# Kernel tuning notes

Hardware: AMD Instinct MI355X
Metric: run time of the kernel (lower is better)

Reference implementation:

```python
import jax, jax.numpy as jnp
import numpy as np

LN_EPS = 1e-5  # torch LayerNorm default
K_NN = 5       # top-5 nearest patterns (simple-surprise path)


def setup_inputs() -> dict:
    key = jax.random.key(0)
    ks = jax.random.split(key, 5)
    B, S, D, M = 8, 8192, 256, 50
    return {
        "hidden_states": jax.random.normal(ks[0], (B, S, D), dtype=jnp.float32),
        "memory": jax.random.normal(ks[1], (M, D), dtype=jnp.float32),
        "W1": jax.random.normal(ks[2], (D, 2 * D), dtype=jnp.float32) * (1.0 / np.sqrt(D)),
        "b1": jnp.zeros((2 * D,), dtype=jnp.float32),
        "W2": jax.random.normal(ks[3], (2 * D, D), dtype=jnp.float32) * (1.0 / np.sqrt(2 * D)),
        "b2": jnp.zeros((D,), dtype=jnp.float32),
        "ln_gamma": jnp.ones((D,), dtype=jnp.float32),
        "ln_beta": jnp.zeros((D,), dtype=jnp.float32),
    }


def reference(hidden_states, memory, W1, b1, W2, b2, ln_gamma, ln_beta):
    # Feature extractor: Linear -> ReLU -> (Dropout, eval=identity) -> Linear -> LayerNorm
    h = jax.nn.relu(jnp.einsum("bsd,de->bse", hidden_states, W1) + b1)
    f = jnp.einsum("bse,ed->bsd", h, W2) + b2
    mu = jnp.mean(f, axis=-1, keepdims=True)
    var = jnp.var(f, axis=-1, keepdims=True)
    feats = (f - mu) * jax.lax.rsqrt(var + LN_EPS) * ln_gamma + ln_beta  # [B,S,D]

    # Simple-surprise path, vectorized over all (b, s) tokens:
    # L2 distance of each token feature to every memory pattern.
    f_sq = jnp.sum(feats * feats, axis=-1)      # [B,S]
    m_sq = jnp.sum(memory * memory, axis=-1)    # [M]
    dots = jnp.einsum("bsd,md->bsm", feats, memory)  # [B,S,M]
    d2 = jnp.maximum(f_sq[..., None] + m_sq - 2.0 * dots, 0.0)
    dists = jnp.sqrt(d2)                        # [B,S,M]

    # k smallest distances -> mean -> sigmoid(avg - 1)
    neg_knn, _ = jax.lax.top_k(-dists, K_NN)    # [B,S,K]
    avg_dist = -jnp.mean(neg_knn, axis=-1)      # [B,S]
    surprise_scores = jax.nn.sigmoid(avg_dist - 1.0)
    return surprise_scores
```

## Files before the change

kernel.cpp:

```cpp
#include <hip/hip_runtime.h>
#include <math.h>

typedef __attribute__((ext_vector_type(8))) short bf16x8;
typedef __attribute__((ext_vector_type(4))) float f32x4;

static __device__ __forceinline__ unsigned int cvtpk(float lo, float hi) {
  unsigned int r;
  asm("v_cvt_pk_bf16_f32 %0, %1, %2" : "=v"(r) : "v"(lo), "v"(hi));
  return r;
}

__global__ void prep_weights(const float* __restrict__ W1,
                             const float* __restrict__ W2,
                             const float* __restrict__ mem,
                             unsigned short* __restrict__ W1T,
                             unsigned short* __restrict__ W2T,
                             unsigned short* __restrict__ memB,
                             float* __restrict__ msq) {
  const int bid = blockIdx.x, tid = threadIdx.x;
  if (bid < 64) {
    __shared__ float tile[64][65];
    const float* src;
    unsigned short* dst;
    int C, Cd, k0, n0;
    if (bid < 32) {
      src = W1; dst = W1T; C = 512; Cd = 256;
      k0 = (bid >> 3) * 64; n0 = (bid & 7) * 64;
    } else {
      int t = bid - 32;
      src = W2; dst = W2T; C = 256; Cd = 512;
      k0 = (t >> 2) * 64; n0 = (t & 3) * 64;
    }
    int r = tid >> 2, c4 = (tid & 3) * 16;
    const float4* s4 = (const float4*)(src + (k0 + r) * C + n0 + c4);
#pragma unroll
    for (int j = 0; j < 4; ++j) {
      float4 v = s4[j];
      tile[r][c4 + j * 4 + 0] = v.x;
      tile[r][c4 + j * 4 + 1] = v.y;
      tile[r][c4 + j * 4 + 2] = v.z;
      tile[r][c4 + j * 4 + 3] = v.w;
    }
    __syncthreads();
    int nl = tid >> 2, kq = (tid & 3) * 16;
    unsigned int o[8];
#pragma unroll
    for (int j = 0; j < 8; ++j)
      o[j] = cvtpk(tile[kq + 2 * j][nl], tile[kq + 2 * j + 1][nl]);
    unsigned short* dp = dst + (n0 + nl) * Cd + k0 + kq;
    *(uint4*)(dp) = make_uint4(o[0], o[1], o[2], o[3]);
    *(uint4*)(dp + 8) = make_uint4(o[4], o[5], o[6], o[7]);
  } else if (bid == 64) {
    int j0 = tid * 64;
#pragma unroll
    for (int j = 0; j < 16; ++j) {
      int e = j0 + j * 4;
      int rrow = e >> 8;
      uint2 w;
      if (rrow < 50) {
        float4 v = *(const float4*)(mem + e);
        w = make_uint2(cvtpk(v.x, v.y), cvtpk(v.z, v.w));
      } else {
        w = make_uint2(0u, 0u);
      }
      *(uint2*)(memB + e) = w;
    }
  } else {
    int rrow = tid >> 2, c0 = (tid & 3) * 64;
    float s = 0.f;
    if (rrow < 50) {
      const float4* m4 = (const float4*)(mem + rrow * 256 + c0);
#pragma unroll
      for (int c = 0; c < 16; ++c) {
        float4 v = m4[c];
        s += v.x * v.x + v.y * v.y + v.z * v.z + v.w * v.w;
      }
    }
    s += __shfl_xor(s, 1, 64);
    s += __shfl_xor(s, 2, 64);
    if ((tid & 3) == 0) msq[rrow] = (rrow < 50) ? s : 1e30f;
  }
}

#define DPitch 53
#define SWZ(b, r) ((b) ^ (((r) & 7) << 4))

__global__ __launch_bounds__(512, 4) void fused_main(
    const float* __restrict__ X, const float* __restrict__ b1v,
    const float* __restrict__ b2v, const float* __restrict__ gammav,
    const float* __restrict__ betav, const unsigned short* __restrict__ W1T,
    const unsigned short* __restrict__ W2T,
    const unsigned short* __restrict__ memB, const float* __restrict__ msq,
    float* __restrict__ out) {
  __shared__ __align__(16) char smem[65536];
  float* distS = (float*)smem;
  float* red = (float*)(smem + 32768);
  float* psum   = red;
  float* psumsq = red + 512;
  float* fsqp   = red + 1024;
  float* muS    = red + 1536;
  float* rstdS  = red + 1600;
  float* fsqS   = red + 1664;

  const char* W1Tc = (const char*)W1T;
  const char* W2Tc = (const char*)W2T;

  const int tid = threadIdx.x;
  const int wid = tid >> 6;
  const int lane = tid & 63;
  const int l16 = lane & 15;
  const int quad = lane >> 4;

  const float4* X4 = (const float4*)(X + (size_t)blockIdx.x * 64 * 256);
#pragma unroll
  for (int j = 0; j < 8; ++j) {
    int row = j * 8 + wid;
    float4 v = X4[row * 64 + lane];
    *(uint2*)(smem + SWZ(row * 512 + lane * 8, row)) =
        make_uint2(cvtpk(v.x, v.y), cvtpk(v.z, v.w));
  }

  f32x4 acc2[2][4];
#pragma unroll
  for (int mt = 0; mt < 2; ++mt) {
    const float4 bb = *(const float4*)(&b2v[wid * 32 + mt * 16 + quad * 4]);
#pragma unroll
    for (int nt = 0; nt < 4; ++nt) {
      acc2[mt][nt][0] = bb.x; acc2[mt][nt][1] = bb.y;
      acc2[mt][nt][2] = bb.z; acc2[mt][nt][3] = bb.w;
    }
  }

  __syncthreads();

#pragma unroll
  for (int cc = 0; cc < 4; ++cc) {
    if (cc > 0) {
      const char* HsR = smem + 32768 + ((cc - 1) & 1) * 16384;
#pragma unroll
      for (int k2 = 0; k2 < 4; ++k2) {
        bf16x8 a[2], b[4];
#pragma unroll
        for (int mt = 0; mt < 2; ++mt)
          a[mt] = *(const bf16x8*)(W2Tc + (wid * 32 + mt * 16 + l16) * 1024 +
                                   (cc - 1) * 256 + k2 * 64 + quad * 16);
#pragma unroll
        for (int nt = 0; nt < 4; ++nt) {
          int r = nt * 16 + l16;
          b[nt] = *(const bf16x8*)(HsR + SWZ(r * 256 + k2 * 64 + quad * 16, r));
        }
#pragma unroll
        for (int mt = 0; mt < 2; ++mt)
#pragma unroll
          for (int nt = 0; nt < 4; ++nt)
            acc2[mt][nt] = __builtin_amdgcn_mfma_f32_16x16x32_bf16(
                a[mt], b[nt], acc2[mt][nt], 0, 0, 0);
      }
    }

    int hbase = cc * 128 + wid * 16;
    f32x4 acc1[4];
    {
      const float4 bb = *(const float4*)(&b1v[hbase + quad * 4]);
#pragma unroll
      for (int nt = 0; nt < 4; ++nt) {
        acc1[nt][0] = bb.x; acc1[nt][1] = bb.y;
        acc1[nt][2] = bb.z; acc1[nt][3] = bb.w;
      }
    }
#pragma unroll
    for (int kk = 0; kk < 8; ++kk) {
      int kb = kk * 64 + quad * 16;
      bf16x8 a = *(const bf16x8*)(W1Tc + (hbase + l16) * 512 + kb);
      bf16x8 b[4];
#pragma unroll
      for (int nt = 0; nt < 4; ++nt) {
        int r = nt * 16 + l16;
        b[nt] = *(const bf16x8*)(smem + SWZ(r * 512 + kb, r));
      }
#pragma unroll
      for (int nt = 0; nt < 4; ++nt)
        acc1[nt] = __builtin_amdgcn_mfma_f32_16x16x32_bf16(a, b[nt], acc1[nt], 0, 0, 0);
    }
    {
      char* HsW = smem + 32768 + (cc & 1) * 16384;
#pragma unroll
      for (int nt = 0; nt < 4; ++nt) {
        int token = nt * 16 + l16;
        f32x4 v = acc1[nt];
        *(uint2*)(HsW + SWZ(token * 256 + wid * 32 + quad * 8, token)) =
            make_uint2(cvtpk(fmaxf(v[0], 0.f), fmaxf(v[1], 0.f)),
                       cvtpk(fmaxf(v[2], 0.f), fmaxf(v[3], 0.f)));
      }
    }
    __syncthreads();
  }

  {
    const char* HsR = smem + 32768 + 16384;
#pragma unroll
    for (int k2 = 0; k2 < 4; ++k2) {
      bf16x8 a[2], b[4];
#pragma unroll
      for (int mt = 0; mt < 2; ++mt)
        a[mt] = *(const bf16x8*)(W2Tc + (wid * 32 + mt * 16 + l16) * 1024 +
                                 3 * 256 + k2 * 64 + quad * 16);
#pragma unroll
      for (int nt = 0; nt < 4; ++nt) {
        int r = nt * 16 + l16;
        b[nt] = *(const bf16x8*)(HsR + SWZ(r * 256 + k2 * 64 + quad * 16, r));
      }
#pragma unroll
      for (int mt = 0; mt < 2; ++mt)
#pragma unroll
        for (int nt = 0; nt < 4; ++nt)
          acc2[mt][nt] = __builtin_amdgcn_mfma_f32_16x16x32_bf16(
              a[mt], b[nt], acc2[mt][nt], 0, 0, 0);
    }
  }

#pragma unroll
  for (int nt = 0; nt < 4; ++nt) {
    float s = 0.f, sq = 0.f;
#pragma unroll
    for (int mt = 0; mt < 2; ++mt)
#pragma unroll
      for (int r = 0; r < 4; ++r) {
        float v = acc2[mt][nt][r];
        s += v; sq += v * v;
      }
    s += __shfl_xor(s, 16, 64); sq += __shfl_xor(sq, 16, 64);
    s += __shfl_xor(s, 32, 64); sq += __shfl_xor(sq, 32, 64);
    if (quad == 0) {
      psum[wid * 64 + nt * 16 + l16] = s;
      psumsq[wid * 64 + nt * 16 + l16] = sq;
    }
  }
  __syncthreads();
  if (tid < 64) {
    float s = 0.f, sq = 0.f;
#pragma unroll
    for (int w = 0; w < 8; ++w) {
      s += psum[w * 64 + tid];
      sq += psumsq[w * 64 + tid];
    }
    float mu = s * (1.f / 256.f);
    float var = sq * (1.f / 256.f) - mu * mu;
    muS[tid] = mu;
    rstdS[tid] = rsqrtf(var + 1e-5f);
  }
  __syncthreads();

  {
    float4 g[2], be_[2];
#pragma unroll
    for (int mt = 0; mt < 2; ++mt) {
      g[mt]   = *(const float4*)(&gammav[wid * 32 + mt * 16 + quad * 4]);
      be_[mt] = *(const float4*)(&betav[wid * 32 + mt * 16 + quad * 4]);
    }
#pragma unroll
    for (int nt = 0; nt < 4; ++nt) {
      int token = nt * 16 + l16;
      float mu = muS[token], rs = rstdS[token];
      float fs = 0.f;
#pragma unroll
      for (int mt = 0; mt < 2; ++mt) {
        float y0 = (acc2[mt][nt][0] - mu) * rs * g[mt].x + be_[mt].x;
        float y1 = (acc2[mt][nt][1] - mu) * rs * g[mt].y + be_[mt].y;
        float y2 = (acc2[mt][nt][2] - mu) * rs * g[mt].z + be_[mt].z;
        float y3 = (acc2[mt][nt][3] - mu) * rs * g[mt].w + be_[mt].w;
        fs += y0 * y0 + y1 * y1 + y2 * y2 + y3 * y3;
        *(uint2*)(smem + SWZ(token * 512 + wid * 64 + mt * 32 + quad * 8, token)) =
            make_uint2(cvtpk(y0, y1), cvtpk(y2, y3));
      }
      fs += __shfl_xor(fs, 16, 64);
      fs += __shfl_xor(fs, 32, 64);
      if (quad == 0) fsqp[wid * 64 + token] = fs;
    }
  }
  __syncthreads();
  if (tid < 64) {
    float fs = 0.f;
#pragma unroll
    for (int w = 0; w < 8; ++w) fs += fsqp[w * 64 + tid];
    fsqS[tid] = fs;
  }
  __syncthreads();

  {
    const int th = wid & 3, mh = wid >> 2;
    f32x4 acc3[2];
#pragma unroll
    for (int j = 0; j < 2; ++j) {
      acc3[j][0] = 0.f; acc3[j][1] = 0.f; acc3[j][2] = 0.f; acc3[j][3] = 0.f;
    }
    const int ar = th * 16 + l16;
#pragma unroll
    for (int kk = 0; kk < 8; ++kk) {
      int kb = kk * 64 + quad * 16;
      bf16x8 a = *(const bf16x8*)(smem + SWZ(ar * 512 + kb, ar));
      int k0 = kk * 32 + quad * 8;
#pragma unroll
      for (int j = 0; j < 2; ++j) {
        bf16x8 b = *(const bf16x8*)(memB + (mh * 32 + j * 16 + l16) * 256 + k0);
        acc3[j] = __builtin_amdgcn_mfma_f32_16x16x32_bf16(a, b, acc3[j], 0, 0, 0);
      }
    }
    __syncthreads();
    float4 fsq4 = *(const float4*)(&fsqS[th * 16 + quad * 4]);
#pragma unroll
    for (int j = 0; j < 2; ++j) {
      int col = mh * 32 + j * 16 + l16;
      float mq = msq[col];
#pragma unroll
      for (int r = 0; r < 4; ++r) {
        float fv = (r == 0) ? fsq4.x : (r == 1) ? fsq4.y : (r == 2) ? fsq4.z : fsq4.w;
        float d2 = fv + mq - 2.f * acc3[j][r];
        float d = sqrtf(fmaxf(d2, 0.f));
        int row = th * 16 + quad * 4 + r;
        if (col < 50) distS[row * DPitch + col] = d;
      }
    }
  }
  __syncthreads();

  if (tid < 64) {
    float b0 = 1e30f, b1 = 1e30f, b2 = 1e30f, b3 = 1e30f, b4 = 1e30f;
    const float* dr = &distS[tid * DPitch];
    for (int j = 0; j < 50; ++j) {
      float v = dr[j];
      b4 = fminf(b4, v);
      float t;
      if (b4 < b3) { t = b3; b3 = b4; b4 = t; }
      if (b3 < b2) { t = b2; b2 = b3; b3 = t; }
      if (b2 < b1) { t = b1; b1 = b2; b2 = t; }
      if (b1 < b0) { t = b0; b0 = b1; b1 = t; }
    }
    float avg = (b0 + b1 + b2 + b3 + b4) * 0.2f;
    float sarg = avg - 1.f;
    out[blockIdx.x * 64 + tid] = 1.f / (1.f + __expf(-sarg));
  }
}

extern "C" void kernel_launch(void* const* d_in, const int* in_sizes, int n_in,
                              void* d_out, int out_size, void* d_ws, size_t ws_size,
                              hipStream_t stream) {
  const float* X   = (const float*)d_in[0];
  const float* mem = (const float*)d_in[1];
  const float* W1  = (const float*)d_in[2];
  const float* b1  = (const float*)d_in[3];
  const float* W2  = (const float*)d_in[4];
  const float* b2  = (const float*)d_in[5];
  const float* g   = (const float*)d_in[6];
  const float* be  = (const float*)d_in[7];
  float* out = (float*)d_out;

  unsigned short* W1T  = (unsigned short*)d_ws;
  unsigned short* W2T  = W1T + 131072;
  unsigned short* memB = W2T + 131072;
  float* msq = (float*)(memB + 16384);

  prep_weights<<<66, 256, 0, stream>>>(W1, W2, mem, W1T, W2T, memB, msq);
  fused_main<<<1024, 512, 0, stream>>>(X, b1, b2, g, be, W1T, W2T, memB, msq, out);
}
```

Baseline: 194.2 us.

## Use 4 waves per block with larger per-wave MFMA tiles and prefetched W2

Halves the block to 256 threads so each wave computes twice as many output rows in both GEMMs, which raises operand reuse per LDS load. W2 fragments for each chunk are loaded into registers ahead of the first GEMM, and the second GEMM now runs right after the barrier of the same chunk, with s_setprio raised around it. The separate reduction steps for LayerNorm stats and feature norms are folded into the consumers, removing two barriers. This costs much higher register pressure (a 64-register W2 prefetch plus larger accumulators) and fewer waves per CU, which could reduce latency hiding.

After: 214.2 us. 1.1x slower.

```diff
diff --git a/kernel.cpp b/kernel.cpp
--- a/kernel.cpp
+++ b/kernel.cpp
@@ -85,7 +85,7 @@
 #define DPitch 53
 #define SWZ(b, r) ((b) ^ (((r) & 7) << 4))
 
-__global__ __launch_bounds__(512, 4) void fused_main(
+__global__ __launch_bounds__(256, 2) void fused_main(
     const float* __restrict__ X, const float* __restrict__ b1v,
     const float* __restrict__ b2v, const float* __restrict__ gammav,
     const float* __restrict__ betav, const unsigned short* __restrict__ W1T,
@@ -96,11 +96,8 @@
   float* distS = (float*)smem;
   float* red = (float*)(smem + 32768);
   float* psum   = red;
-  float* psumsq = red + 512;
-  float* fsqp   = red + 1024;
-  float* muS    = red + 1536;
-  float* rstdS  = red + 1600;
-  float* fsqS   = red + 1664;
+  float* psumsq = red + 256;
+  float* fsqp   = red + 512;
 
   const char* W1Tc = (const char*)W1T;
   const char* W2Tc = (const char*)W2T;
@@ -113,17 +110,17 @@
 
   const float4* X4 = (const float4*)(X + (size_t)blockIdx.x * 64 * 256);
 #pragma unroll
-  for (int j = 0; j < 8; ++j) {
-    int row = j * 8 + wid;
+  for (int j = 0; j < 16; ++j) {
+    int row = j * 4 + wid;
     float4 v = X4[row * 64 + lane];
     *(uint2*)(smem + SWZ(row * 512 + lane * 8, row)) =
         make_uint2(cvtpk(v.x, v.y), cvtpk(v.z, v.w));
   }
 
-  f32x4 acc2[2][4];
-#pragma unroll
-  for (int mt = 0; mt < 2; ++mt) {
-    const float4 bb = *(const float4*)(&b2v[wid * 32 + mt * 16 + quad * 4]);
+  f32x4 acc2[4][4];
+#pragma unroll
+  for (int mt = 0; mt < 4; ++mt) {
+    const float4 bb = *(const float4*)(&b2v[wid * 64 + mt * 16 + quad * 4]);
 #pragma unroll
     for (int nt = 0; nt < 4; ++nt) {
       acc2[mt][nt][0] = bb.x; acc2[mt][nt][1] = bb.y;
@@ -135,87 +132,77 @@
 
 #pragma unroll
   for (int cc = 0; cc < 4; ++cc) {
-    if (cc > 0) {
-      const char* HsR = smem + 32768 + ((cc - 1) & 1) * 16384;
+    bf16x8 a2p[4][4];
+#pragma unroll
+    for (int k2 = 0; k2 < 4; ++k2)
+#pragma unroll
+      for (int mt = 0; mt < 4; ++mt)
+        a2p[k2][mt] = *(const bf16x8*)(W2Tc + (wid * 64 + mt * 16 + l16) * 1024 +
+                                       cc * 256 + k2 * 64 + quad * 16);
+
+    int hbase = cc * 128 + wid * 32;
+    f32x4 acc1[2][4];
+#pragma unroll
+    for (int mt = 0; mt < 2; ++mt) {
+      const float4 bb = *(const float4*)(&b1v[hbase + mt * 16 + quad * 4]);
+#pragma unroll
+      for (int nt = 0; nt < 4; ++nt) {
+        acc1[mt][nt][0] = bb.x; acc1[mt][nt][1] = bb.y;
+        acc1[mt][nt][2] = bb.z; acc1[mt][nt][3] = bb.w;
+      }
+    }
+#pragma unroll
+    for (int kk = 0; kk < 8; ++kk) {
+      int kb = kk * 64 + quad * 16;
+      bf16x8 a[2], b[4];
+#pragma unroll
+      for (int mt = 0; mt < 2; ++mt)
+        a[mt] = *(const bf16x8*)(W1Tc + (hbase + mt * 16 + l16) * 512 + kb);
+#pragma unroll
+      for (int nt = 0; nt < 4; ++nt) {
+        int r = nt * 16 + l16;
+        b[nt] = *(const bf16x8*)(smem + SWZ(r * 512 + kb, r));
+      }
+#pragma unroll
+      for (int mt = 0; mt < 2; ++mt)
+#pragma unroll
+        for (int nt = 0; nt < 4; ++nt)
+          acc1[mt][nt] = __builtin_amdgcn_mfma_f32_16x16x32_bf16(
+              a[mt], b[nt], acc1[mt][nt], 0, 0, 0);
+    }
+    {
+      char* HsW = smem + 32768 + (cc & 1) * 16384;
+#pragma unroll
+      for (int mt = 0; mt < 2; ++mt)
+#pragma unroll
+        for (int nt = 0; nt < 4; ++nt) {
+          int token = nt * 16 + l16;
+          f32x4 v = acc1[mt][nt];
+          *(uint2*)(HsW + SWZ(token * 256 + wid * 64 + mt * 32 + quad * 8, token)) =
+              make_uint2(cvtpk(fmaxf(v[0], 0.f), fmaxf(v[1], 0.f)),
+                         cvtpk(fmaxf(v[2], 0.f), fmaxf(v[3], 0.f)));
+        }
+    }
+    __syncthreads();
+    {
+      const char* HsR = smem + 32768 + (cc & 1) * 16384;
+      __builtin_amdgcn_s_setprio(1);
 #pragma unroll
       for (int k2 = 0; k2 < 4; ++k2) {
-        bf16x8 a[2], b[4];
-#pragma unroll
-        for (int mt = 0; mt < 2; ++mt)
-          a[mt] = *(const bf16x8*)(W2Tc + (wid * 32 + mt * 16 + l16) * 1024 +
-                                   (cc - 1) * 256 + k2 * 64 + quad * 16);
+        bf16x8 b[4];
 #pragma unroll
         for (int nt = 0; nt < 4; ++nt) {
           int r = nt * 16 + l16;
           b[nt] = *(const bf16x8*)(HsR + SWZ(r * 256 + k2 * 64 + quad * 16, r));
         }
 #pragma unroll
-        for (int mt = 0; mt < 2; ++mt)
+        for (int mt = 0; mt < 4; ++mt)
 #pragma unroll
           for (int nt = 0; nt < 4; ++nt)
             acc2[mt][nt] = __builtin_amdgcn_mfma_f32_16x16x32_bf16(
-                a[mt], b[nt], acc2[mt][nt], 0, 0, 0);
-      }
-    }
-
-    int hbase = cc * 128 + wid * 16;
-    f32x4 acc1[4];
-    {
-      const float4 bb = *(const float4*)(&b1v[hbase + quad * 4]);
-#pragma unroll
-      for (int nt = 0; nt < 4; ++nt) {
-        acc1[nt][0] = bb.x; acc1[nt][1] = bb.y;
-        acc1[nt][2] = bb.z; acc1[nt][3] = bb.w;
-      }
-    }
-#pragma unroll
-    for (int kk = 0; kk < 8; ++kk) {
-      int kb = kk * 64 + quad * 16;
-      bf16x8 a = *(const bf16x8*)(W1Tc + (hbase + l16) * 512 + kb);
-      bf16x8 b[4];
-#pragma unroll
-      for (int nt = 0; nt < 4; ++nt) {
-        int r = nt * 16 + l16;
-        b[nt] = *(const bf16x8*)(smem + SWZ(r * 512 + kb, r));
-      }
-#pragma unroll
-      for (int nt = 0; nt < 4; ++nt)
-        acc1[nt] = __builtin_amdgcn_mfma_f32_16x16x32_bf16(a, b[nt], acc1[nt], 0, 0, 0);
-    }
-    {
-      char* HsW = smem + 32768 + (cc & 1) * 16384;
-#pragma unroll
-      for (int nt = 0; nt < 4; ++nt) {
-        int token = nt * 16 + l16;
-        f32x4 v = acc1[nt];
-        *(uint2*)(HsW + SWZ(token * 256 + wid * 32 + quad * 8, token)) =
-            make_uint2(cvtpk(fmaxf(v[0], 0.f), fmaxf(v[1], 0.f)),
-                       cvtpk(fmaxf(v[2], 0.f), fmaxf(v[3], 0.f)));
-      }
-    }
-    __syncthreads();
-  }
-
-  {
-    const char* HsR = smem + 32768 + 16384;
-#pragma unroll
-    for (int k2 = 0; k2 < 4; ++k2) {
-      bf16x8 a[2], b[4];
-#pragma unroll
-      for (int mt = 0; mt < 2; ++mt)
-        a[mt] = *(const bf16x8*)(W2Tc + (wid * 32 + mt * 16 + l16) * 1024 +
-                                 3 * 256 + k2 * 64 + quad * 16);
-#pragma unroll
-      for (int nt = 0; nt < 4; ++nt) {
-        int r = nt * 16 + l16;
-        b[nt] = *(const bf16x8*)(HsR + SWZ(r * 256 + k2 * 64 + quad * 16, r));
-      }
-#pragma unroll
-      for (int mt = 0; mt < 2; ++mt)
-#pragma unroll
-        for (int nt = 0; nt < 4; ++nt)
-          acc2[mt][nt] = __builtin_amdgcn_mfma_f32_16x16x32_bf16(
-              a[mt], b[nt], acc2[mt][nt], 0, 0, 0);
+                a2p[k2][mt], b[nt], acc2[mt][nt], 0, 0, 0);
+      }
+      __builtin_amdgcn_s_setprio(0);
     }
   }
 
@@ -223,7 +210,7 @@
   for (int nt = 0; nt < 4; ++nt) {
     float s = 0.f, sq = 0.f;
 #pragma unroll
-    for (int mt = 0; mt < 2; ++mt)
+    for (int mt = 0; mt < 4; ++mt)
 #pragma unroll
       for (int r = 0; r < 4; ++r) {
         float v = acc2[mt][nt][r];
@@ -237,40 +224,30 @@
     }
   }
   __syncthreads();
-  if (tid < 64) {
-    float s = 0.f, sq = 0.f;
-#pragma unroll
-    for (int w = 0; w < 8; ++w) {
-      s += psum[w * 64 + tid];
-      sq += psumsq[w * 64 + tid];
-    }
-    float mu = s * (1.f / 256.f);
-    float var = sq * (1.f / 256.f) - mu * mu;
-    muS[tid] = mu;
-    rstdS[tid] = rsqrtf(var + 1e-5f);
-  }
-  __syncthreads();
 
   {
-    float4 g[2], be_[2];
-#pragma unroll
-    for (int mt = 0; mt < 2; ++mt) {
-      g[mt]   = *(const float4*)(&gammav[wid * 32 + mt * 16 + quad * 4]);
-      be_[mt] = *(const float4*)(&betav[wid * 32 + mt * 16 + quad * 4]);
+    float4 g[4], be_[4];
+#pragma unroll
+    for (int mt = 0; mt < 4; ++mt) {
+      g[mt]   = *(const float4*)(&gammav[wid * 64 + mt * 16 + quad * 4]);
+      be_[mt] = *(const float4*)(&betav[wid * 64 + mt * 16 + quad * 4]);
     }
 #pragma unroll
     for (int nt = 0; nt < 4; ++nt) {
       int token = nt * 16 + l16;
-      float mu = muS[token], rs = rstdS[token];
+      float s  = psum[token] + psum[64 + token] + psum[128 + token] + psum[192 + token];
+      float sq = psumsq[token] + psumsq[64 + token] + psumsq[128 + token] + psumsq[192 + token];
+      float mu = s * (1.f / 256.f);
+      float rs = rsqrtf(sq * (1.f / 256.f) - mu * mu + 1e-5f);
       float fs = 0.f;
 #pragma unroll
-      for (int mt = 0; mt < 2; ++mt) {
+      for (int mt = 0; mt < 4; ++mt) {
         float y0 = (acc2[mt][nt][0] - mu) * rs * g[mt].x + be_[mt].x;
         float y1 = (acc2[mt][nt][1] - mu) * rs * g[mt].y + be_[mt].y;
         float y2 = (acc2[mt][nt][2] - mu) * rs * g[mt].z + be_[mt].z;
         float y3 = (acc2[mt][nt][3] - mu) * rs * g[mt].w + be_[mt].w;
         fs += y0 * y0 + y1 * y1 + y2 * y2 + y3 * y3;
-        *(uint2*)(smem + SWZ(token * 512 + wid * 64 + mt * 32 + quad * 8, token)) =
+        *(uint2*)(smem + SWZ(token * 512 + wid * 128 + mt * 32 + quad * 8, token)) =
             make_uint2(cvtpk(y0, y1), cvtpk(y2, y3));
       }
       fs += __shfl_xor(fs, 16, 64);
@@ -279,45 +256,41 @@
     }
   }
   __syncthreads();
-  if (tid < 64) {
-    float fs = 0.f;
-#pragma unroll
-    for (int w = 0; w < 8; ++w) fs += fsqp[w * 64 + tid];
-    fsqS[tid] = fs;
-  }
-  __syncthreads();
-
+
+  f32x4 acc3[4];
+#pragma unroll
+  for (int nt = 0; nt < 4; ++nt) {
+    acc3[nt][0] = 0.f; acc3[nt][1] = 0.f; acc3[nt][2] = 0.f; acc3[nt][3] = 0.f;
+  }
+#pragma unroll
+  for (int kk = 0; kk < 8; ++kk) {
+    int kb = kk * 64 + quad * 16;
+    int ar = wid * 16 + l16;
+    bf16x8 a = *(const bf16x8*)(smem + SWZ(ar * 512 + kb, ar));
+    int k0 = kk * 32 + quad * 8;
+#pragma unroll
+    for (int nt = 0; nt < 4; ++nt) {
+      bf16x8 b = *(const bf16x8*)(memB + (nt * 16 + l16) * 256 + k0);
+      acc3[nt] = __builtin_amdgcn_mfma_f32_16x16x32_bf16(a, b, acc3[nt], 0, 0, 0);
+    }
+  }
+  __syncthreads();
   {
-    const int th = wid & 3, mh = wid >> 2;
-    f32x4 acc3[2];
-#pragma unroll
-    for (int j = 0; j < 2; ++j) {
-      acc3[j][0] = 0.f; acc3[j][1] = 0.f; acc3[j][2] = 0.f; acc3[j][3] = 0.f;
-    }
-    const int ar = th * 16 + l16;
-#pragma unroll
-    for (int kk = 0; kk < 8; ++kk) {
-      int kb = kk * 64 + quad * 16;
-      bf16x8 a = *(const bf16x8*)(smem + SWZ(ar * 512 + kb, ar));
-      int k0 = kk * 32 + quad * 8;
-#pragma unroll
-      for (int j = 0; j < 2; ++j) {
-        bf16x8 b = *(const bf16x8*)(memB + (mh * 32 + j * 16 + l16) * 256 + k0);
-        acc3[j] = __builtin_amdgcn_mfma_f32_16x16x32_bf16(a, b, acc3[j], 0, 0, 0);
-      }
-    }
-    __syncthreads();
-    float4 fsq4 = *(const float4*)(&fsqS[th * 16 + quad * 4]);
-#pragma unroll
-    for (int j = 0; j < 2; ++j) {
-      int col = mh * 32 + j * 16 + l16;
+    float fv[4];
+#pragma unroll
+    for (int r = 0; r < 4; ++r) {
+      int row = wid * 16 + quad * 4 + r;
+      fv[r] = fsqp[row] + fsqp[64 + row] + fsqp[128 + row] + fsqp[192 + row];
+    }
+#pragma unroll
+    for (int nt = 0; nt < 4; ++nt) {
+      int col = nt * 16 + l16;
       float mq = msq[col];
 #pragma unroll
       for (int r = 0; r < 4; ++r) {
-        float fv = (r == 0) ? fsq4.x : (r == 1) ? fsq4.y : (r == 2) ? fsq4.z : fsq4.w;
-        float d2 = fv + mq - 2.f * acc3[j][r];
+        float d2 = fv[r] + mq - 2.f * acc3[nt][r];
         float d = sqrtf(fmaxf(d2, 0.f));
-        int row = th * 16 + quad * 4 + r;
+        int row = wid * 16 + quad * 4 + r;
         if (col < 50) distS[row * DPitch + col] = d;
       }
     }
@@ -361,5 +334,5 @@
   float* msq = (float*)(memB + 16384);
 
   prep_weights<<<66, 256, 0, stream>>>(W1, W2, mem, W1T, W2T, memB, msq);
-  fused_main<<<1024, 512, 0, stream>>>(X, b1, b2, g, be, W1T, W2T, memB, msq, out);
+  fused_main<<<1024, 256, 0, stream>>>(X, b1, b2, g, be, W1T, W2T, memB, msq, out);
 }
```

## Remove reduction barriers, rotate hidden-chunk order, raise MFMA priority

Applied to the files above, without the earlier changes.

Drops the single-wave LayerNorm and feature-norm reductions along with their extra barriers. Every wave now sums the per-wave partials from shared memory itself, and the distance buffer is moved so it no longer overlaps the bf16 features, which removes another barrier. Blocks also rotate the order in which they process the hidden chunks so they do not all read the same weight rows at once, and the W2 MFMA phases run under a raised wave priority. Launch bounds are relaxed to 2 blocks per SM, giving more register headroom at the risk of lower occupancy. The cost is redundant LDS reads for the per-token sums.

Result: slower. 199.5 us (+2.7%).

```diff
diff --git a/kernel.cpp b/kernel.cpp
--- a/kernel.cpp
+++ b/kernel.cpp
@@ -85,7 +85,7 @@
 #define DPitch 53
 #define SWZ(b, r) ((b) ^ (((r) & 7) << 4))
 
-__global__ __launch_bounds__(512, 4) void fused_main(
+__global__ __launch_bounds__(512, 2) void fused_main(
     const float* __restrict__ X, const float* __restrict__ b1v,
     const float* __restrict__ b2v, const float* __restrict__ gammav,
     const float* __restrict__ betav, const unsigned short* __restrict__ W1T,
@@ -93,14 +93,11 @@
     const unsigned short* __restrict__ memB, const float* __restrict__ msq,
     float* __restrict__ out) {
   __shared__ __align__(16) char smem[65536];
-  float* distS = (float*)smem;
   float* red = (float*)(smem + 32768);
   float* psum   = red;
   float* psumsq = red + 512;
   float* fsqp   = red + 1024;
-  float* muS    = red + 1536;
-  float* rstdS  = red + 1600;
-  float* fsqS   = red + 1664;
+  float* distS = (float*)(smem + 49152);
 
   const char* W1Tc = (const char*)W1T;
   const char* W2Tc = (const char*)W2T;
@@ -133,17 +130,23 @@
 
   __syncthreads();
 
+  const int rot = blockIdx.x & 3;
+
 #pragma unroll
   for (int cc = 0; cc < 4; ++cc) {
+    const int ccr = (cc + rot) & 3;
+    const int cpr = ((cc - 1) + rot) & 3;
+
     if (cc > 0) {
       const char* HsR = smem + 32768 + ((cc - 1) & 1) * 16384;
+      __builtin_amdgcn_s_setprio(1);
 #pragma unroll
       for (int k2 = 0; k2 < 4; ++k2) {
         bf16x8 a[2], b[4];
 #pragma unroll
         for (int mt = 0; mt < 2; ++mt)
           a[mt] = *(const bf16x8*)(W2Tc + (wid * 32 + mt * 16 + l16) * 1024 +
-                                   (cc - 1) * 256 + k2 * 64 + quad * 16);
+                                   cpr * 256 + k2 * 64 + quad * 16);
 #pragma unroll
         for (int nt = 0; nt < 4; ++nt) {
           int r = nt * 16 + l16;
@@ -156,9 +159,10 @@
             acc2[mt][nt] = __builtin_amdgcn_mfma_f32_16x16x32_bf16(
                 a[mt], b[nt], acc2[mt][nt], 0, 0, 0);
       }
-    }
-
-    int hbase = cc * 128 + wid * 16;
+      __builtin_amdgcn_s_setprio(0);
+    }
+
+    int hbase = ccr * 128 + wid * 16;
     f32x4 acc1[4];
     {
       const float4 bb = *(const float4*)(&b1v[hbase + quad * 4]);
@@ -197,14 +201,16 @@
   }
 
   {
+    const int cpr = (3 + rot) & 3;
     const char* HsR = smem + 32768 + 16384;
+    __builtin_amdgcn_s_setprio(1);
 #pragma unroll
     for (int k2 = 0; k2 < 4; ++k2) {
       bf16x8 a[2], b[4];
 #pragma unroll
       for (int mt = 0; mt < 2; ++mt)
         a[mt] = *(const bf16x8*)(W2Tc + (wid * 32 + mt * 16 + l16) * 1024 +
-                                 3 * 256 + k2 * 64 + quad * 16);
+                                 cpr * 256 + k2 * 64 + quad * 16);
 #pragma unroll
       for (int nt = 0; nt < 4; ++nt) {
         int r = nt * 16 + l16;
@@ -217,6 +223,7 @@
           acc2[mt][nt] = __builtin_amdgcn_mfma_f32_16x16x32_bf16(
               a[mt], b[nt], acc2[mt][nt], 0, 0, 0);
     }
+    __builtin_amdgcn_s_setprio(0);
   }
 
 #pragma unroll
@@ -237,19 +244,6 @@
     }
   }
   __syncthreads();
-  if (tid < 64) {
-    float s = 0.f, sq = 0.f;
-#pragma unroll
-    for (int w = 0; w < 8; ++w) {
-      s += psum[w * 64 + tid];
-      sq += psumsq[w * 64 + tid];
-    }
-    float mu = s * (1.f / 256.f);
-    float var = sq * (1.f / 256.f) - mu * mu;
-    muS[tid] = mu;
-    rstdS[tid] = rsqrtf(var + 1e-5f);
-  }
-  __syncthreads();
 
   {
     float4 g[2], be_[2];
@@ -261,7 +255,14 @@
 #pragma unroll
     for (int nt = 0; nt < 4; ++nt) {
       int token = nt * 16 + l16;
-      float mu = muS[token], rs = rstdS[token];
+      float s = 0.f, sq = 0.f;
+#pragma unroll
+      for (int w = 0; w < 8; ++w) {
+        s += psum[w * 64 + token];
+        sq += psumsq[w * 64 + token];
+      }
+      float mu = s * (1.f / 256.f);
+      float rs = rsqrtf(sq * (1.f / 256.f) - mu * mu + 1e-5f);
       float fs = 0.f;
 #pragma unroll
       for (int mt = 0; mt < 2; ++mt) {
@@ -279,13 +280,6 @@
     }
   }
   __syncthreads();
-  if (tid < 64) {
-    float fs = 0.f;
-#pragma unroll
-    for (int w = 0; w < 8; ++w) fs += fsqp[w * 64 + tid];
-    fsqS[tid] = fs;
-  }
-  __syncthreads();
 
   {
     const int th = wid & 3, mh = wid >> 2;
@@ -306,16 +300,22 @@
         acc3[j] = __builtin_amdgcn_mfma_f32_16x16x32_bf16(a, b, acc3[j], 0, 0, 0);
       }
     }
-    __syncthreads();
-    float4 fsq4 = *(const float4*)(&fsqS[th * 16 + quad * 4]);
+    float fv[4];
+#pragma unroll
+    for (int r = 0; r < 4; ++r) {
+      int row = th * 16 + quad * 4 + r;
+      float fs = 0.f;
+#pragma unroll
+      for (int w = 0; w < 8; ++w) fs += fsqp[w * 64 + row];
+      fv[r] = fs;
+    }
 #pragma unroll
     for (int j = 0; j < 2; ++j) {
       int col = mh * 32 + j * 16 + l16;
       float mq = msq[col];
 #pragma unroll
       for (int r = 0; r < 4; ++r) {
-        float fv = (r == 0) ? fsq4.x : (r == 1) ? fsq4.y : (r == 2) ? fsq4.z : fsq4.w;
-        float d2 = fv + mq - 2.f * acc3[j][r];
+        float d2 = fv[r] + mq - 2.f * acc3[j][r];
         float d = sqrtf(fmaxf(d2, 0.f));
         int row = th * 16 + quad * 4 + r;
         if (col < 50) distS[row * DPitch + col] = d;
```
